# Kernel tuning notes

Measured on AMD Instinct MI355X. Metric: run time of the kernel, lower is better.

The kernel has to match this reference:

```python
import jax, jax.numpy as jnp
import numpy as np

# dims
B, T, HORIZON, N = 32, 12, 12, 512
IN, OUT, H, P = 1, 1, 64, 32
S, ML, MG, DE = 12, 64, 32, 10  # S_local == S_global


def setup_inputs() -> dict:
    key = jax.random.key(0)
    ks = jax.random.split(key, 12)
    f = lambda k, shp: jax.random.normal(k, shp, dtype=jnp.float32)
    return {
        "source": f(ks[0], (B, T, N, IN)),
        "local_mem": f(ks[1], (ML, S, P)) * 0.1,
        "global_mem": f(ks[2], (MG, S, P)) * 0.1,
        "Wq": f(ks[3], (H, P)) / np.sqrt(H),
        "bq": jnp.zeros((P,), jnp.float32),
        "node_emb": f(ks[4], (N, DE)) * 0.1,
        "weight_pool": f(ks[5], (DE, 2 * P, H)) / np.sqrt(2 * P),
        "Wz": f(ks[6], (IN + H, H)) / np.sqrt(IN + H), "bz": jnp.zeros((H,), jnp.float32),
        "Wr": f(ks[7], (IN + H, H)) / np.sqrt(IN + H), "br": jnp.zeros((H,), jnp.float32),
        "Wc": f(ks[8], (IN + H, H)) / np.sqrt(IN + H), "bc": jnp.zeros((H,), jnp.float32),
        "Wo": f(ks[9], (H, OUT)) / np.sqrt(H), "bo": jnp.zeros((OUT,), jnp.float32),
    }


def _forward(source, local_mem, global_mem, Wq, bq, node_emb, weight_pool,
             Wz, bz, Wr, br, Wc, bc, Wo, bo):
    b, t, n, _ = source.shape
    hdim = Wz.shape[1]
    s = local_mem.shape[1]
    # node-specific hypernetwork weights: [N, 2P, H]
    nsw = jnp.einsum('nd,dfh->nfh', node_emb, weight_pool)
    lmean = local_mem.mean(axis=1)   # [ML, P]
    gmean = global_mem.mean(axis=1)  # [MG, P]

    def dcn(buffer):  # buffer: [B, N, S, H]
        q = jnp.einsum('bnsh,hp->bnsp', buffer, Wq) + bq          # [B,N,S,P]
        a_l = jax.nn.softmax(jnp.einsum('bnsp,msp->bnm', q, local_mem), axis=-1)
        a_g = jax.nn.softmax(jnp.einsum('bnsp,msp->bnm', q, global_mem), axis=-1)
        # context mean over S == attn @ mean-over-S memory
        lc = a_l @ lmean                                           # [B,N,P]
        gc = a_g @ gmean                                           # [B,N,P]
        fused = jnp.concatenate([lc, gc], axis=-1)                 # [B,N,2P]
        return jnp.einsum('bnf,nfh->bnh', fused, nsw)              # [B,N,H]

    def cell(x_t, h_prev, buffer):
        ctx = dcn(buffer)
        comb = jnp.concatenate([x_t, h_prev], axis=-1)
        z = jax.nn.sigmoid(comb @ Wz + bz)
        r = jax.nn.sigmoid(comb @ Wr + br)
        comb2 = jnp.concatenate([x_t, r * h_prev], axis=-1)
        hc = jnp.tanh(comb2 @ Wc + bc + ctx)
        return (1.0 - z) * h_prev + z * hc

    h0 = jnp.zeros((b, n, hdim), source.dtype)
    buf0 = jnp.zeros((b, n, s, hdim), source.dtype)

    def enc_step(carry, x_t):
        h, buf = carry
        h = cell(x_t, h, buf)
        buf = jax.lax.stop_gradient(
            jnp.concatenate([buf[:, :, 1:], h[:, :, None]], axis=2))
        return (h, buf), None

    (h, buf), _ = jax.lax.scan(enc_step, (h0, buf0), jnp.moveaxis(source, 1, 0))

    def dec_step(carry, _):
        h, buf, x = carry
        h = cell(x, h, buf)
        buf = jax.lax.stop_gradient(
            jnp.concatenate([buf[:, :, 1:], h[:, :, None]], axis=2))
        y = h @ Wo + bo
        return (h, buf, y), y

    _, ys = jax.lax.scan(dec_step, (h, buf, source[:, -1]), None, length=HORIZON)
    return jnp.moveaxis(ys, 0, 1)  # [B, horizon, N, OUT]


def reference(source, local_mem, global_mem, Wq, bq, node_emb, weight_pool,
              Wz, bz, Wr, br, Wc, bc, Wo, bo):
    return _forward(source, local_mem, global_mem, Wq, bq, node_emb, weight_pool,
                    Wz, bz, Wr, br, Wc, bc, Wo, bo)
```

## Files before the change

kernel.cpp:

```cpp
#include <hip/hip_runtime.h>


typedef short short8 __attribute__((ext_vector_type(8)));
typedef float f32x4 __attribute__((ext_vector_type(4)));

#define DEV static __device__ __forceinline__

DEV unsigned short f2bf(float f) {
  union { float f; unsigned u; } v; v.f = f;
  unsigned r = v.u + 0x7FFFu + ((v.u >> 16) & 1u);
  return (unsigned short)(r >> 16);
}
DEV float bf2f(unsigned short b) {
  union { unsigned u; float f; } v; v.u = ((unsigned)b) << 16;
  return v.f;
}
DEV unsigned cvtpk(float a, float b) {
  unsigned r;
  asm("v_cvt_pk_bf16_f32 %0, %1, %2" : "=v"(r) : "v"(a), "v"(b));
  return r;
}
DEV float rcpf(float x) { return __builtin_amdgcn_rcpf(x); }

#define WG_OFF  36864
#define WQ_OFF  61440
#define LM_OFF  63488
#define GM_OFF  65536
#define WS_TOT  66560

#define L_WLO   73728
#define L_LM    98304
#define L_SCR   104448
#define SCR_STRIDE 13312
#define SMEM_BYTES 157696

#define R_AL 0
#define R_AG 2048
#define R_FU 3072
#define R_HH 5120
#define R_HL 7168
#define R_RH 9216
#define R_RL 11264
#define R_NH 0
#define R_QQ 2048

#define MFMA16(a, b, c) __builtin_amdgcn_mfma_f32_16x16x32_bf16((a), (b), (c), 0, 0, 0)

DEV int scat_off(int col, int g) {
  int kp = col & 31;
  return ((col >> 5) << 10) + ((kp >> 3) << 8) + (g << 6) + ((kp & 7) << 1);
}
DEV void scat4(char* p, f32x4 v) {
  unsigned p0 = cvtpk(v[0], v[1]), p1 = cvtpk(v[2], v[3]);
  *(unsigned short*)(p)      = (unsigned short)p0;
  *(unsigned short*)(p + 16) = (unsigned short)(p0 >> 16);
  *(unsigned short*)(p + 32) = (unsigned short)p1;
  *(unsigned short*)(p + 48) = (unsigned short)(p1 >> 16);
}
DEV void scat4_hilo(char* ph, char* pl, f32x4 v) {
  unsigned p0 = cvtpk(v[0], v[1]), p1 = cvtpk(v[2], v[3]);
  float h0 = __uint_as_float(p0 << 16), h1 = __uint_as_float(p0 & 0xFFFF0000u);
  float h2 = __uint_as_float(p1 << 16), h3 = __uint_as_float(p1 & 0xFFFF0000u);
  unsigned q0 = cvtpk(v[0] - h0, v[1] - h1), q1 = cvtpk(v[2] - h2, v[3] - h3);
  *(unsigned short*)(ph)      = (unsigned short)p0;
  *(unsigned short*)(ph + 16) = (unsigned short)(p0 >> 16);
  *(unsigned short*)(ph + 32) = (unsigned short)p1;
  *(unsigned short*)(ph + 48) = (unsigned short)(p1 >> 16);
  *(unsigned short*)(pl)      = (unsigned short)q0;
  *(unsigned short*)(pl + 16) = (unsigned short)(q0 >> 16);
  *(unsigned short*)(pl + 32) = (unsigned short)q1;
  *(unsigned short*)(pl + 48) = (unsigned short)(q1 >> 16);
}

__global__ __launch_bounds__(256, 1) void dyna_prep(
    const float* __restrict__ lmem, const float* __restrict__ gmem,
    const float* __restrict__ Wq, const float* __restrict__ Wz,
    const float* __restrict__ Wr, const float* __restrict__ Wc,
    unsigned short* __restrict__ ws)
{
  int i = blockIdx.x * 256 + threadIdx.x;
  if (i >= WS_TOT) return;

  if (i < WG_OFF) {
    int f = i >> 9, r = i & 511, lane = r >> 3, j = r & 7;
    int g = lane >> 4, u = lane & 15;
    int s = f / 6, nt = f % 6;
    int m = nt * 16 + u, p = g * 8 + j;
    float v = (m < 64) ? lmem[(m * 12 + s) * 32 + p]
                       : gmem[((m - 64) * 12 + s) * 32 + p];
    ws[i] = f2bf(v);
  } else if (i < WQ_OFF) {
    int t = i - WG_OFF;
    int f = t >> 9, r = t & 511, lane = r >> 3, j = r & 7;
    int g = lane >> 4, u = lane & 15;
    int hl = f & 1, kc = (f >> 1) & 1, nt = (f >> 2) & 3, gate = f >> 4;
    int k = kc * 32 + g * 8 + j, col = nt * 16 + u;
    const float* W = (gate == 0) ? Wz : (gate == 1) ? Wr : Wc;
    float w = W[(1 + k) * 64 + col];
    if (hl) { float hi = bf2f(f2bf(w)); ws[i] = f2bf(w - hi); }
    else ws[i] = f2bf(w);
  } else if (i < LM_OFF) {
    int t = i - WQ_OFF;
    int f = t >> 9, r = t & 511, lane = r >> 3, j = r & 7;
    int g = lane >> 4, u = lane & 15;
    int kc = f & 1, nt = f >> 1;
    int k = kc * 32 + g * 8 + j, col = nt * 16 + u;
    ws[i] = f2bf(Wq[k * 32 + col]);
  } else if (i < GM_OFF) {
    int t = i - LM_OFF;
    int f = t >> 9, r = t & 511, lane = r >> 3, j = r & 7;
    int g = lane >> 4, u = lane & 15;
    int kc = f >> 1, nt = f & 1;
    int k = kc * 32 + g * 8 + j, p = nt * 16 + u;
    float s = 0.f;
    for (int ss = 0; ss < 12; ++ss) s += lmem[(k * 12 + ss) * 32 + p];
    ws[i] = f2bf(s * (1.0f / 12.0f));
  } else {
    int t = i - GM_OFF;
    int f = t >> 9, r = t & 511, lane = r >> 3, j = r & 7;
    int g = lane >> 4, u = lane & 15;
    int nt = f;
    int k = g * 8 + j, p = nt * 16 + u;
    float s = 0.f;
    for (int ss = 0; ss < 12; ++ss) s += gmem[(k * 12 + ss) * 32 + p];
    ws[i] = f2bf(s * (1.0f / 12.0f));
  }
}

__global__ __launch_bounds__(256, 1) void dyna_main(
    const float* __restrict__ src, const float* __restrict__ emb,
    const float* __restrict__ pool, const float* __restrict__ bq,
    const float* __restrict__ Wz, const float* __restrict__ bz,
    const float* __restrict__ Wr, const float* __restrict__ br,
    const float* __restrict__ Wc, const float* __restrict__ bc,
    const float* __restrict__ Wo, const float* __restrict__ bo,
    const unsigned short* __restrict__ ws, float* __restrict__ out)
{
  extern __shared__ char smem[];
  const int tid = threadIdx.x;
  const int lane = tid & 63, wid = tid >> 6;
  const int g = lane >> 4, u = lane & 15;
  const int n = blockIdx.x * 2 + (wid >> 1);
  const int hb = wid & 1;

  {
    const short8* s8 = (const short8*)ws;
    short8* d8 = (short8*)smem;
    for (int i = tid; i < 6528; i += 256) {
      int s;
      if (i < 4608) s = i;
      else if (i < 6144) {
        int r = i - 4608;
        s = 4608 + ((r >> 6) << 7) + 64 + (r & 63);
      } else s = 7936 + (i - 6144);
      d8[i] = s8[s];
    }
  }

  short8 whf[3][2][4];
  #pragma unroll
  for (int gate = 0; gate < 3; ++gate)
    #pragma unroll
    for (int kc = 0; kc < 2; ++kc)
      #pragma unroll
      for (int nt = 0; nt < 4; ++nt) {
        int f = ((gate * 4 + nt) * 2 + kc) * 2;
        whf[gate][kc][nt] = *(const short8*)(ws + WG_OFF + f * 512 + lane * 8);
      }
  short8 wqf[2][2];
  #pragma unroll
  for (int kc = 0; kc < 2; ++kc)
    #pragma unroll
    for (int nt = 0; nt < 2; ++nt)
      wqf[kc][nt] = *(const short8*)(ws + WQ_OFF + (nt * 2 + kc) * 512 + lane * 8);

  short8 nswf[2][4];
  #pragma unroll
  for (int kc = 0; kc < 2; ++kc)
    #pragma unroll
    for (int nt = 0; nt < 4; ++nt) {
      short8 v;
      #pragma unroll
      for (int j = 0; j < 8; ++j) {
        int k = kc * 32 + g * 8 + j, col = nt * 16 + u;
        float s = 0.f;
        #pragma unroll
        for (int d = 0; d < 10; ++d)
          s += emb[n * 10 + d] * pool[(d * 64 + k) * 64 + col];
        v[j] = (short)f2bf(s);
      }
      nswf[kc][nt] = v;
    }

  float w0z[4], w0r[4], w0c[4], bzv[4], brv[4], bcv[4], wov[4], bqv[2];
  #pragma unroll
  for (int nt = 0; nt < 4; ++nt) {
    int col = nt * 16 + u;
    w0z[nt] = Wz[col]; w0r[nt] = Wr[col]; w0c[nt] = Wc[col];
    bzv[nt] = bz[col]; brv[nt] = br[col]; bcv[nt] = bc[col];
    wov[nt] = Wo[col];
  }
  bqv[0] = bq[u]; bqv[1] = bq[16 + u];
  const float bov = bo[0];

  char* SCR = smem + L_SCR + wid * SCR_STRIDE;

  short8 qh[12];
  {
    short8 qi;
    #pragma unroll
    for (int j = 0; j < 8; ++j) qi[j] = (short)f2bf(bq[g * 8 + j]);
    #pragma unroll
    for (int s = 0; s < 12; ++s) qh[s] = qi;
  }
  f32x4 hreg[4];
  #pragma unroll
  for (int nt = 0; nt < 4; ++nt) hreg[nt] = (f32x4){0.f, 0.f, 0.f, 0.f};
  float xreg[4] = {0.f, 0.f, 0.f, 0.f};

  __syncthreads();

  for (int t = 0; t < 24; ++t) {
    if (t <= 12) {
      int tt = t < 12 ? t : 11;
      #pragma unroll
      for (int reg = 0; reg < 4; ++reg) {
        int b = hb * 16 + g * 4 + reg;
        xreg[reg] = src[(b * 12 + tt) * 512 + n];
      }
    }

    #pragma unroll
    for (int nt = 0; nt < 4; ++nt) {
      int so = scat_off(nt * 16 + u, g);
      scat4_hilo(SCR + R_HH + so, SCR + R_HL + so, hreg[nt]);
    }

    f32x4 sacc[6];
    #pragma unroll
    for (int nt = 0; nt < 6; ++nt) sacc[nt] = (f32x4){0.f, 0.f, 0.f, 0.f};
    __builtin_amdgcn_s_setprio(1);
    #pragma unroll
    for (int s = 0; s < 12; ++s) {
      #pragma unroll
      for (int nt = 0; nt < 6; ++nt) {
        short8 bf = *(const short8*)(smem + ((s * 6 + nt) << 10) + (lane << 4));
        sacc[nt] = MFMA16(qh[s], bf, sacc[nt]);
      }
    }
    __builtin_amdgcn_s_setprio(0);

    short8 hhi0 = *(const short8*)(SCR + R_HH + (lane << 4));
    short8 hhi1 = *(const short8*)(SCR + R_HH + 1024 + (lane << 4));
    short8 hlo0 = *(const short8*)(SCR + R_HL + (lane << 4));
    short8 hlo1 = *(const short8*)(SCR + R_HL + 1024 + (lane << 4));
    f32x4 zacc[4], racc[4];
    #pragma unroll
    for (int nt = 0; nt < 4; ++nt) {
      zacc[nt] = (f32x4){0.f, 0.f, 0.f, 0.f};
      racc[nt] = (f32x4){0.f, 0.f, 0.f, 0.f};
    }
    #pragma unroll
    for (int kc = 0; kc < 2; ++kc) {
      short8 hh = kc ? hhi1 : hhi0;
      short8 hl = kc ? hlo1 : hlo0;
      #pragma unroll
      for (int nt = 0; nt < 4; ++nt) {
        short8 wzl = *(const short8*)(smem + L_WLO + (((0 * 4 + nt) * 2 + kc) << 10) + (lane << 4));
        short8 wrl = *(const short8*)(smem + L_WLO + (((1 * 4 + nt) * 2 + kc) << 10) + (lane << 4));
        zacc[nt] = MFMA16(hh, whf[0][kc][nt], zacc[nt]);
        zacc[nt] = MFMA16(hl, whf[0][kc][nt], zacc[nt]);
        zacc[nt] = MFMA16(hh, wzl, zacc[nt]);
        racc[nt] = MFMA16(hh, whf[1][kc][nt], racc[nt]);
        racc[nt] = MFMA16(hl, whf[1][kc][nt], racc[nt]);
        racc[nt] = MFMA16(hh, wrl, racc[nt]);
      }
    }

    #pragma unroll
    for (int nt = 0; nt < 6; ++nt)
      #pragma unroll
      for (int reg = 0; reg < 4; ++reg)
        sacc[nt][reg] = __expf(sacc[nt][reg]);
    float invl[4], invg[4];
    #pragma unroll
    for (int reg = 0; reg < 4; ++reg) {
      float sl = (sacc[0][reg] + sacc[1][reg]) + (sacc[2][reg] + sacc[3][reg]);
      sl += __shfl_xor(sl, 1); sl += __shfl_xor(sl, 2);
      sl += __shfl_xor(sl, 4); sl += __shfl_xor(sl, 8);
      invl[reg] = rcpf(sl);
      float sg = sacc[4][reg] + sacc[5][reg];
      sg += __shfl_xor(sg, 1); sg += __shfl_xor(sg, 2);
      sg += __shfl_xor(sg, 4); sg += __shfl_xor(sg, 8);
      invg[reg] = rcpf(sg);
    }

    #pragma unroll
    for (int nt = 0; nt < 4; ++nt)
      scat4(SCR + R_AL + scat_off(nt * 16 + u, g), sacc[nt]);
    #pragma unroll
    for (int nt = 0; nt < 2; ++nt)
      scat4(SCR + R_AG + scat_off(nt * 16 + u, g), sacc[4 + nt]);

    #pragma unroll
    for (int nt = 0; nt < 4; ++nt)
      #pragma unroll
      for (int reg = 0; reg < 4; ++reg) {
        float zv = zacc[nt][reg] + xreg[reg] * w0z[nt] + bzv[nt];
        zacc[nt][reg] = rcpf(1.0f + __expf(-zv));
        float rv = racc[nt][reg] + xreg[reg] * w0r[nt] + brv[nt];
        racc[nt][reg] = rcpf(1.0f + __expf(-rv));
      }

    #pragma unroll
    for (int nt = 0; nt < 4; ++nt) {
      int so = scat_off(nt * 16 + u, g);
      f32x4 rh;
      #pragma unroll
      for (int reg = 0; reg < 4; ++reg) rh[reg] = racc[nt][reg] * hreg[nt][reg];
      scat4_hilo(SCR + R_RH + so, SCR + R_RL + so, rh);
    }

    short8 alf0 = *(const short8*)(SCR + R_AL + (lane << 4));
    short8 alf1 = *(const short8*)(SCR + R_AL + 1024 + (lane << 4));
    short8 agf  = *(const short8*)(SCR + R_AG + (lane << 4));
    f32x4 lacc[2], gacc[2];
    #pragma unroll
    for (int nt = 0; nt < 2; ++nt) {
      lacc[nt] = (f32x4){0.f, 0.f, 0.f, 0.f};
      gacc[nt] = (f32x4){0.f, 0.f, 0.f, 0.f};
      short8 lm0 = *(const short8*)(smem + L_LM + ((0 * 2 + nt) << 10) + (lane << 4));
      short8 lm1 = *(const short8*)(smem + L_LM + ((1 * 2 + nt) << 10) + (lane << 4));
      short8 gm  = *(const short8*)(smem + L_LM + 4096 + (nt << 10) + (lane << 4));
      lacc[nt] = MFMA16(alf0, lm0, lacc[nt]);
      lacc[nt] = MFMA16(alf1, lm1, lacc[nt]);
      gacc[nt] = MFMA16(agf, gm, gacc[nt]);
    }

    short8 rhh0 = *(const short8*)(SCR + R_RH + (lane << 4));
    short8 rhh1 = *(const short8*)(SCR + R_RH + 1024 + (lane << 4));
    short8 rhl0 = *(const short8*)(SCR + R_RL + (lane << 4));
    short8 rhl1 = *(const short8*)(SCR + R_RL + 1024 + (lane << 4));
    f32x4 hacc[4];
    #pragma unroll
    for (int nt = 0; nt < 4; ++nt) hacc[nt] = (f32x4){0.f, 0.f, 0.f, 0.f};
    #pragma unroll
    for (int kc = 0; kc < 2; ++kc) {
      short8 hh = kc ? rhh1 : rhh0;
      short8 hl = kc ? rhl1 : rhl0;
      #pragma unroll
      for (int nt = 0; nt < 4; ++nt) {
        short8 wcl = *(const short8*)(smem + L_WLO + (((2 * 4 + nt) * 2 + kc) << 10) + (lane << 4));
        hacc[nt] = MFMA16(hh, whf[2][kc][nt], hacc[nt]);
        hacc[nt] = MFMA16(hl, whf[2][kc][nt], hacc[nt]);
        hacc[nt] = MFMA16(hh, wcl, hacc[nt]);
      }
    }

    #pragma unroll
    for (int nt = 0; nt < 2; ++nt) {
      f32x4 lv, gv;
      #pragma unroll
      for (int reg = 0; reg < 4; ++reg) {
        lv[reg] = lacc[nt][reg] * invl[reg];
        gv[reg] = gacc[nt][reg] * invg[reg];
      }
      scat4(SCR + R_FU + scat_off(nt * 16 + u, g), lv);
      scat4(SCR + R_FU + scat_off(32 + nt * 16 + u, g), gv);
    }
    short8 fuf0 = *(const short8*)(SCR + R_FU + (lane << 4));
    short8 fuf1 = *(const short8*)(SCR + R_FU + 1024 + (lane << 4));

    f32x4 cacc[4];
    #pragma unroll
    for (int nt = 0; nt < 4; ++nt) {
      cacc[nt] = (f32x4){0.f, 0.f, 0.f, 0.f};
      cacc[nt] = MFMA16(fuf0, nswf[0][nt], cacc[nt]);
      cacc[nt] = MFMA16(fuf1, nswf[1][nt], cacc[nt]);
    }

    #pragma unroll
    for (int nt = 0; nt < 4; ++nt)
      #pragma unroll
      for (int reg = 0; reg < 4; ++reg) {
        float pv = hacc[nt][reg] + cacc[nt][reg] + xreg[reg] * w0c[nt] + bcv[nt];
        float tdenom = rcpf(1.0f + __expf(2.0f * pv));
        float hc = 1.0f - 2.0f * tdenom;
        float zv = zacc[nt][reg];
        hreg[nt][reg] = (1.0f - zv) * hreg[nt][reg] + zv * hc;
      }

    #pragma unroll
    for (int nt = 0; nt < 4; ++nt)
      scat4(SCR + R_NH + scat_off(nt * 16 + u, g), hreg[nt]);
    short8 nh0 = *(const short8*)(SCR + R_NH + (lane << 4));
    short8 nh1 = *(const short8*)(SCR + R_NH + 1024 + (lane << 4));

    f32x4 qacc[2];
    #pragma unroll
    for (int nt = 0; nt < 2; ++nt) {
      qacc[nt] = (f32x4){0.f, 0.f, 0.f, 0.f};
      qacc[nt] = MFMA16(nh0, wqf[0][nt], qacc[nt]);
      qacc[nt] = MFMA16(nh1, wqf[1][nt], qacc[nt]);
      #pragma unroll
      for (int reg = 0; reg < 4; ++reg) qacc[nt][reg] += bqv[nt];
    }
    #pragma unroll
    for (int nt = 0; nt < 2; ++nt)
      scat4(SCR + R_QQ + scat_off(nt * 16 + u, g), qacc[nt]);
    short8 qnf = *(const short8*)(SCR + R_QQ + (lane << 4));
    #pragma unroll
    for (int s = 0; s < 11; ++s) qh[s] = qh[s + 1];
    qh[11] = qnf;

    if (t >= 12) {
      #pragma unroll
      for (int reg = 0; reg < 4; ++reg) {
        float yp = hreg[0][reg] * wov[0] + hreg[1][reg] * wov[1] +
                   hreg[2][reg] * wov[2] + hreg[3][reg] * wov[3];
        yp += __shfl_xor(yp, 1); yp += __shfl_xor(yp, 2);
        yp += __shfl_xor(yp, 4); yp += __shfl_xor(yp, 8);
        float yv = yp + bov;
        xreg[reg] = yv;
        if (u == 0) {
          int b = hb * 16 + g * 4 + reg;
          out[(b * 12 + (t - 12)) * 512 + n] = yv;
        }
      }
    }
  }
}

extern "C" void kernel_launch(void* const* d_in, const int* in_sizes, int n_in,
                              void* d_out, int out_size, void* d_ws, size_t ws_size,
                              hipStream_t stream) {
  const float* src  = (const float*)d_in[0];
  const float* lmem = (const float*)d_in[1];
  const float* gmem = (const float*)d_in[2];
  const float* Wq   = (const float*)d_in[3];
  const float* bq   = (const float*)d_in[4];
  const float* emb  = (const float*)d_in[5];
  const float* pool = (const float*)d_in[6];
  const float* Wz   = (const float*)d_in[7];
  const float* bz   = (const float*)d_in[8];
  const float* Wr   = (const float*)d_in[9];
  const float* br   = (const float*)d_in[10];
  const float* Wc   = (const float*)d_in[11];
  const float* bc   = (const float*)d_in[12];
  const float* Wo   = (const float*)d_in[13];
  const float* bo   = (const float*)d_in[14];
  float* out = (float*)d_out;
  unsigned short* ws = (unsigned short*)d_ws;

  dyna_prep<<<260, 256, 0, stream>>>(lmem, gmem, Wq, Wz, Wr, Wc, ws);

  (void)hipFuncSetAttribute((const void*)dyna_main,
                            hipFuncAttributeMaxDynamicSharedMemorySize,
                            SMEM_BYTES);
  dyna_main<<<256, 256, SMEM_BYTES, stream>>>(src, emb, pool, bq, Wz, bz, Wr, br,
                                              Wc, bc, Wo, bo, ws, out);
}
```

Baseline: 235.1 us.

## Keep memory fragments in registers and move gate weights to LDS

The 72 memory-score B fragments (local and global memories) now stay in registers, and the hi/lo gate weights, Wq and the per-node hypernetwork weights are read from LDS instead. This removes the LDS reads from the 12×6 score MFMA loop, which is on the critical path of each recurrent step. The new h hi/lo scatter is reused both for Wq and for the next step's gates, which removes one scatter per step. In exchange it adds LDS traffic in the gate GEMMs and raises register pressure (72 short8 registers), which could cause spills or lower occupancy.

```diff
diff --git a/kernel.cpp b/kernel.cpp
--- a/kernel.cpp
+++ b/kernel.cpp
@@ -28,11 +28,12 @@
 #define GM_OFF  65536
 #define WS_TOT  66560
 
-#define L_WLO   73728
-#define L_LM    98304
-#define L_SCR   104448
-#define SCR_STRIDE 13312
-#define SMEM_BYTES 157696
+#define L_W     0
+#define L_WQ    49152
+#define L_LM    53248
+#define L_SCR   59392
+#define SCR_STRIDE 21504
+#define SMEM_BYTES 145408
 
 #define R_AL 0
 #define R_AG 2048
@@ -41,8 +42,8 @@
 #define R_HL 7168
 #define R_RH 9216
 #define R_RL 11264
-#define R_NH 0
-#define R_QQ 2048
+#define R_NSW 13312
+#define R_QQ 0
 
 #define MFMA16(a, b, c) __builtin_amdgcn_mfma_f32_16x16x32_bf16((a), (b), (c), 0, 0, 0)
 
@@ -146,35 +147,16 @@
   {
     const short8* s8 = (const short8*)ws;
     short8* d8 = (short8*)smem;
-    for (int i = tid; i < 6528; i += 256) {
-      int s;
-      if (i < 4608) s = i;
-      else if (i < 6144) {
-        int r = i - 4608;
-        s = 4608 + ((r >> 6) << 7) + 64 + (r & 63);
-      } else s = 7936 + (i - 6144);
-      d8[i] = s8[s];
-    }
-  }
-
-  short8 whf[3][2][4];
+    for (int i = tid; i < 3712; i += 256) d8[i] = s8[4608 + i];
+  }
+
+  short8 marr[72];
   #pragma unroll
-  for (int gate = 0; gate < 3; ++gate)
-    #pragma unroll
-    for (int kc = 0; kc < 2; ++kc)
-      #pragma unroll
-      for (int nt = 0; nt < 4; ++nt) {
-        int f = ((gate * 4 + nt) * 2 + kc) * 2;
-        whf[gate][kc][nt] = *(const short8*)(ws + WG_OFF + f * 512 + lane * 8);
-      }
-  short8 wqf[2][2];
-  #pragma unroll
-  for (int kc = 0; kc < 2; ++kc)
-    #pragma unroll
-    for (int nt = 0; nt < 2; ++nt)
-      wqf[kc][nt] = *(const short8*)(ws + WQ_OFF + (nt * 2 + kc) * 512 + lane * 8);
-
-  short8 nswf[2][4];
+  for (int f = 0; f < 72; ++f)
+    marr[f] = *(const short8*)(ws + (f << 9) + lane * 8);
+
+  char* SCR = smem + L_SCR + wid * SCR_STRIDE;
+
   #pragma unroll
   for (int kc = 0; kc < 2; ++kc)
     #pragma unroll
@@ -189,7 +171,7 @@
           s += emb[n * 10 + d] * pool[(d * 64 + k) * 64 + col];
         v[j] = (short)f2bf(s);
       }
-      nswf[kc][nt] = v;
+      *(short8*)(SCR + R_NSW + ((kc * 4 + nt) << 10) + (lane << 4)) = v;
     }
 
   float w0z[4], w0r[4], w0c[4], bzv[4], brv[4], bcv[4], wov[4], bqv[2];
@@ -203,8 +185,6 @@
   bqv[0] = bq[u]; bqv[1] = bq[16 + u];
   const float bov = bo[0];
 
-  char* SCR = smem + L_SCR + wid * SCR_STRIDE;
-
   short8 qh[12];
   {
     short8 qi;
@@ -218,6 +198,12 @@
   for (int nt = 0; nt < 4; ++nt) hreg[nt] = (f32x4){0.f, 0.f, 0.f, 0.f};
   float xreg[4] = {0.f, 0.f, 0.f, 0.f};
 
+  #pragma unroll
+  for (int nt = 0; nt < 4; ++nt) {
+    int so = scat_off(nt * 16 + u, g);
+    scat4_hilo(SCR + R_HH + so, SCR + R_HL + so, hreg[nt]);
+  }
+
   __syncthreads();
 
   for (int t = 0; t < 24; ++t) {
@@ -229,53 +215,23 @@
         xreg[reg] = src[(b * 12 + tt) * 512 + n];
       }
     }
-
-    #pragma unroll
-    for (int nt = 0; nt < 4; ++nt) {
-      int so = scat_off(nt * 16 + u, g);
-      scat4_hilo(SCR + R_HH + so, SCR + R_HL + so, hreg[nt]);
-    }
-
-    f32x4 sacc[6];
-    #pragma unroll
-    for (int nt = 0; nt < 6; ++nt) sacc[nt] = (f32x4){0.f, 0.f, 0.f, 0.f};
-    __builtin_amdgcn_s_setprio(1);
-    #pragma unroll
-    for (int s = 0; s < 12; ++s) {
-      #pragma unroll
-      for (int nt = 0; nt < 6; ++nt) {
-        short8 bf = *(const short8*)(smem + ((s * 6 + nt) << 10) + (lane << 4));
-        sacc[nt] = MFMA16(qh[s], bf, sacc[nt]);
-      }
-    }
-    __builtin_amdgcn_s_setprio(0);
 
     short8 hhi0 = *(const short8*)(SCR + R_HH + (lane << 4));
     short8 hhi1 = *(const short8*)(SCR + R_HH + 1024 + (lane << 4));
     short8 hlo0 = *(const short8*)(SCR + R_HL + (lane << 4));
     short8 hlo1 = *(const short8*)(SCR + R_HL + 1024 + (lane << 4));
-    f32x4 zacc[4], racc[4];
-    #pragma unroll
-    for (int nt = 0; nt < 4; ++nt) {
-      zacc[nt] = (f32x4){0.f, 0.f, 0.f, 0.f};
-      racc[nt] = (f32x4){0.f, 0.f, 0.f, 0.f};
-    }
-    #pragma unroll
-    for (int kc = 0; kc < 2; ++kc) {
-      short8 hh = kc ? hhi1 : hhi0;
-      short8 hl = kc ? hlo1 : hlo0;
-      #pragma unroll
-      for (int nt = 0; nt < 4; ++nt) {
-        short8 wzl = *(const short8*)(smem + L_WLO + (((0 * 4 + nt) * 2 + kc) << 10) + (lane << 4));
-        short8 wrl = *(const short8*)(smem + L_WLO + (((1 * 4 + nt) * 2 + kc) << 10) + (lane << 4));
-        zacc[nt] = MFMA16(hh, whf[0][kc][nt], zacc[nt]);
-        zacc[nt] = MFMA16(hl, whf[0][kc][nt], zacc[nt]);
-        zacc[nt] = MFMA16(hh, wzl, zacc[nt]);
-        racc[nt] = MFMA16(hh, whf[1][kc][nt], racc[nt]);
-        racc[nt] = MFMA16(hl, whf[1][kc][nt], racc[nt]);
-        racc[nt] = MFMA16(hh, wrl, racc[nt]);
-      }
-    }
+
+    f32x4 sacc[6];
+    #pragma unroll
+    for (int nt = 0; nt < 6; ++nt) sacc[nt] = (f32x4){0.f, 0.f, 0.f, 0.f};
+    __builtin_amdgcn_s_setprio(1);
+    #pragma unroll
+    for (int s = 0; s < 12; ++s) {
+      #pragma unroll
+      for (int nt = 0; nt < 6; ++nt)
+        sacc[nt] = MFMA16(qh[s], marr[s * 6 + nt], sacc[nt]);
+    }
+    __builtin_amdgcn_s_setprio(0);
 
     #pragma unroll
     for (int nt = 0; nt < 6; ++nt)
@@ -302,6 +258,31 @@
     for (int nt = 0; nt < 2; ++nt)
       scat4(SCR + R_AG + scat_off(nt * 16 + u, g), sacc[4 + nt]);
 
+    f32x4 zacc[4], racc[4];
+    #pragma unroll
+    for (int nt = 0; nt < 4; ++nt) {
+      zacc[nt] = (f32x4){0.f, 0.f, 0.f, 0.f};
+      racc[nt] = (f32x4){0.f, 0.f, 0.f, 0.f};
+    }
+    #pragma unroll
+    for (int kc = 0; kc < 2; ++kc) {
+      short8 hh = kc ? hhi1 : hhi0;
+      short8 hl = kc ? hlo1 : hlo0;
+      #pragma unroll
+      for (int nt = 0; nt < 4; ++nt) {
+        short8 wzh = *(const short8*)(smem + L_W + ((((0 + nt) * 2 + kc) * 2 + 0) << 10) + (lane << 4));
+        short8 wzl = *(const short8*)(smem + L_W + ((((0 + nt) * 2 + kc) * 2 + 1) << 10) + (lane << 4));
+        zacc[nt] = MFMA16(hh, wzh, zacc[nt]);
+        zacc[nt] = MFMA16(hl, wzh, zacc[nt]);
+        zacc[nt] = MFMA16(hh, wzl, zacc[nt]);
+        short8 wrh = *(const short8*)(smem + L_W + ((((4 + nt) * 2 + kc) * 2 + 0) << 10) + (lane << 4));
+        short8 wrl = *(const short8*)(smem + L_W + ((((4 + nt) * 2 + kc) * 2 + 1) << 10) + (lane << 4));
+        racc[nt] = MFMA16(hh, wrh, racc[nt]);
+        racc[nt] = MFMA16(hl, wrh, racc[nt]);
+        racc[nt] = MFMA16(hh, wrl, racc[nt]);
+      }
+    }
+
     #pragma unroll
     for (int nt = 0; nt < 4; ++nt)
       #pragma unroll
@@ -350,9 +331,10 @@
       short8 hl = kc ? rhl1 : rhl0;
       #pragma unroll
       for (int nt = 0; nt < 4; ++nt) {
-        short8 wcl = *(const short8*)(smem + L_WLO + (((2 * 4 + nt) * 2 + kc) << 10) + (lane << 4));
-        hacc[nt] = MFMA16(hh, whf[2][kc][nt], hacc[nt]);
-        hacc[nt] = MFMA16(hl, whf[2][kc][nt], hacc[nt]);
+        short8 wch = *(const short8*)(smem + L_W + ((((8 + nt) * 2 + kc) * 2 + 0) << 10) + (lane << 4));
+        short8 wcl = *(const short8*)(smem + L_W + ((((8 + nt) * 2 + kc) * 2 + 1) << 10) + (lane << 4));
+        hacc[nt] = MFMA16(hh, wch, hacc[nt]);
+        hacc[nt] = MFMA16(hl, wch, hacc[nt]);
         hacc[nt] = MFMA16(hh, wcl, hacc[nt]);
       }
     }
@@ -374,9 +356,11 @@
     f32x4 cacc[4];
     #pragma unroll
     for (int nt = 0; nt < 4; ++nt) {
+      short8 nf0 = *(const short8*)(SCR + R_NSW + ((0 * 4 + nt) << 10) + (lane << 4));
+      short8 nf1 = *(const short8*)(SCR + R_NSW + ((1 * 4 + nt) << 10) + (lane << 4));
       cacc[nt] = (f32x4){0.f, 0.f, 0.f, 0.f};
-      cacc[nt] = MFMA16(fuf0, nswf[0][nt], cacc[nt]);
-      cacc[nt] = MFMA16(fuf1, nswf[1][nt], cacc[nt]);
+      cacc[nt] = MFMA16(fuf0, nf0, cacc[nt]);
+      cacc[nt] = MFMA16(fuf1, nf1, cacc[nt]);
     }
 
     #pragma unroll
@@ -391,17 +375,21 @@
       }
 
     #pragma unroll
-    for (int nt = 0; nt < 4; ++nt)
-      scat4(SCR + R_NH + scat_off(nt * 16 + u, g), hreg[nt]);
-    short8 nh0 = *(const short8*)(SCR + R_NH + (lane << 4));
-    short8 nh1 = *(const short8*)(SCR + R_NH + 1024 + (lane << 4));
+    for (int nt = 0; nt < 4; ++nt) {
+      int so = scat_off(nt * 16 + u, g);
+      scat4_hilo(SCR + R_HH + so, SCR + R_HL + so, hreg[nt]);
+    }
+    short8 nh0 = *(const short8*)(SCR + R_HH + (lane << 4));
+    short8 nh1 = *(const short8*)(SCR + R_HH + 1024 + (lane << 4));
 
     f32x4 qacc[2];
     #pragma unroll
     for (int nt = 0; nt < 2; ++nt) {
+      short8 wq0 = *(const short8*)(smem + L_WQ + ((nt * 2 + 0) << 10) + (lane << 4));
+      short8 wq1 = *(const short8*)(smem + L_WQ + ((nt * 2 + 1) << 10) + (lane << 4));
       qacc[nt] = (f32x4){0.f, 0.f, 0.f, 0.f};
-      qacc[nt] = MFMA16(nh0, wqf[0][nt], qacc[nt]);
-      qacc[nt] = MFMA16(nh1, wqf[1][nt], qacc[nt]);
+      qacc[nt] = MFMA16(nh0, wq0, qacc[nt]);
+      qacc[nt] = MFMA16(nh1, wq1, qacc[nt]);
       #pragma unroll
       for (int reg = 0; reg < 4; ++reg) qacc[nt][reg] += bqv[nt];
     }
```

New measurement: 211.9 us. 9.9% less time.
